# Kernel optimization log

Measured on AMD Instinct MI355X. Metric: run time of the kernel, lower is better.

## Reference

```python
import jax, jax.numpy as jnp
import numpy as np

H = 8        # heads
DH = 64      # dim_head
IMG = 32     # image_size
KS = 5       # kernel_size (odd)
SCALE = DH ** -0.5


def _unfold(t, ks):
    # t: (b, c, Hp, Wp) already padded. Returns (b, c*ks*ks, Ho*Wo) with
    # channel-major layout (c outermost, then kh, kw) matching torch F.unfold.
    b, c, Hp, Wp = t.shape
    Ho, Wo = Hp - ks + 1, Wp - ks + 1
    pat = jnp.stack([t[:, :, i:i + Ho, j:j + Wo]
                     for i in range(ks) for j in range(ks)], axis=2)  # (b,c,ks*ks,Ho,Wo)
    return pat.reshape(b, c * ks * ks, Ho * Wo)


def setup_inputs() -> dict:
    key = jax.random.key(0)
    k1, k2, k3, k4 = jax.random.split(key, 4)
    b, n, dim, inner = 2, 1152, 512, 512
    x = jax.random.normal(k1, (b, n, dim), jnp.float32)
    w_qkv = jax.random.normal(k2, (dim, inner * 3), jnp.float32) * 0.02
    w_out = jax.random.normal(k3, (inner, dim), jnp.float32) * 0.02
    b_out = jax.random.normal(k4, (dim,), jnp.float32) * 0.02
    return {"x": x, "w_qkv": w_qkv, "w_out": w_out, "b_out": b_out}


def reference(x, w_qkv, w_out, b_out):
    b, n, dim = x.shape
    img_len = IMG * IMG
    text_len = n - img_len
    NEG = -jnp.finfo(x.dtype).max

    qkv = x @ w_qkv                                   # (b, n, 3*inner)
    q, k, v = jnp.split(qkv, 3, axis=-1)

    def to_heads(t):
        return t.reshape(b, n, H, DH).transpose(0, 2, 1, 3).reshape(b * H, n, DH)

    q = to_heads(q) * SCALE
    k = to_heads(k)
    v = to_heads(v)

    # faithful to source: text slice is t[:, img_seq_len:], image is t[:, -img_seq_len:]
    q_text, q_img = q[:, img_len:], q[:, -img_len:]
    k_text, k_img = k[:, img_len:], k[:, -img_len:]
    v_text, v_img = v[:, img_len:], v[:, -img_len:]

    # ---- text branch. NOTE: source uses non-inplace masked_fill, so the
    # causal mask has NO effect -> plain softmax (faithful reproduction).
    dots_text = jnp.einsum('bid,bjd->bij', q_text, k_text)
    attn_text = jax.nn.softmax(dots_text, axis=-1)
    out_text = jnp.einsum('bij,bjd->bid', attn_text, v_text)

    # ---- image branch: local window via unfold
    def to_loc(t):
        g = t.transpose(0, 2, 1).reshape(b * H, DH, IMG, IMG)
        p = KS // 2
        g = jnp.pad(g, ((0, 0), (0, 0), (p, p), (p, p)))
        u = _unfold(g, KS)  # (bh, DH*KS*KS, img_len), channel-major (d outer)
        # faithful to source rearrange 'b (j d) i -> b i j d' (j outermost),
        # which regroups the channel-major unfold output.
        return u.reshape(b * H, KS * KS, DH, img_len).transpose(0, 3, 1, 2)

    k_loc = to_loc(k_img)  # (bh, img_len, KS*KS, DH)
    v_loc = to_loc(v_img)

    dots_txt = jnp.einsum('bid,bjd->bij', q_img, k_text)     # (bh, img_len, text_len)
    dots_loc = jnp.einsum('bid,bijd->bij', q_img, k_loc)     # (bh, img_len, KS*KS)

    # per-query key index mask (padded positions get index img_len -> never masked)
    p = KS // 2
    idx = jnp.arange(img_len, dtype=jnp.float32).reshape(1, 1, IMG, IMG)
    idx = jnp.pad(idx, ((0, 0), (0, 0), (p, p), (p, p)), constant_values=float(img_len))
    kidx = _unfold(idx, KS).transpose(0, 2, 1)               # (1, img_len, KS*KS)
    qidx = jnp.arange(img_len, dtype=jnp.float32).reshape(1, -1, 1)
    mask_loc = qidx <= kidx                                  # faithful: keep q <= k
    dots_loc = jnp.where(mask_loc, dots_loc, NEG)

    dots_img = jnp.concatenate([dots_txt, dots_loc], axis=-1)
    attn_img = jax.nn.softmax(dots_img, axis=-1)
    out_img = (jnp.einsum('bij,bjd->bid', attn_img[..., :text_len], v_text)
               + jnp.einsum('bij,bijd->bid', attn_img[..., text_len:], v_loc))

    out = jnp.concatenate([out_text, out_img], axis=1)       # (bh, n, DH)
    out = out.reshape(b, H, n, DH).transpose(0, 2, 1, 3).reshape(b, n, H * DH)
    return out @ w_out + b_out
```

## Files before the change

kernel.cpp:

```cpp
#include <hip/hip_runtime.h>
#include <hip/hip_bf16.h>
#include <math.h>

#define NTOK 1152
#define DIM 512
#define NQKV 1536
#define DHEAD 64
#define NBH 16
#define TEXTN 128
#define IMGLEN 1024
#define SEG (NBH * NTOK * DHEAD)
#define STF 68
#define TSTATE_F (NBH * IMGLEN * STF)
#define LPAD 40
#define KTSZ (NBH * TEXTN * DHEAD)

typedef __attribute__((ext_vector_type(8))) short bf16x8;
typedef __attribute__((ext_vector_type(8))) ushort u16x8;
typedef __attribute__((ext_vector_type(4))) float f32x4;

__device__ __forceinline__ ushort f2bf(float f) {
    unsigned u = __float_as_uint(f);
    unsigned r = (u + 0x7FFFu + ((u >> 16) & 1u)) >> 16;
    return (ushort)r;
}
__device__ __forceinline__ float bf2f(ushort u) {
    return __uint_as_float(((unsigned)u) << 16);
}

__global__ __launch_bounds__(256) void prep_x_k(const float* __restrict__ X,
                                                ushort* __restrict__ xhi,
                                                ushort* __restrict__ xlo) {
    int i = (blockIdx.x * 256 + threadIdx.x) * 4;
    float4 v = *(const float4*)(X + i);
    ushort4 h, l;
    h.x = f2bf(v.x); l.x = f2bf(v.x - bf2f(h.x));
    h.y = f2bf(v.y); l.y = f2bf(v.y - bf2f(h.y));
    h.z = f2bf(v.z); l.z = f2bf(v.z - bf2f(h.z));
    h.w = f2bf(v.w); l.w = f2bf(v.w - bf2f(h.w));
    *(ushort4*)(xhi + i) = h;
    *(ushort4*)(xlo + i) = l;
}

__global__ __launch_bounds__(256) void prep_wt_k(const float* __restrict__ W,
                                                 ushort* __restrict__ thi,
                                                 ushort* __restrict__ tlo,
                                                 int K, int N) {
    __shared__ float tile[32][33];
    const int bx = blockIdx.x, by = blockIdx.y;
    const int c = threadIdx.x & 31, r8 = threadIdx.x >> 5;
#pragma unroll
    for (int i = 0; i < 4; ++i) {
        int rr = r8 + i * 8;
        tile[rr][c] = W[(size_t)(by * 32 + rr) * N + bx * 32 + c];
    }
    __syncthreads();
#pragma unroll
    for (int i = 0; i < 4; ++i) {
        int rr = r8 + i * 8;
        float v = tile[c][rr];
        size_t o = (size_t)(bx * 32 + rr) * K + by * 32 + c;
        ushort h = f2bf(v);
        thi[o] = h;
        tlo[o] = f2bf(v - bf2f(h));
    }
}

__global__ __launch_bounds__(256) void gemm_qkv_mfma(const ushort* __restrict__ xhi,
                                                     const ushort* __restrict__ xlo,
                                                     const ushort* __restrict__ wthi,
                                                     const ushort* __restrict__ wtlo,
                                                     float* __restrict__ qh,
                                                     float* __restrict__ kh,
                                                     float* __restrict__ vh,
                                                     ushort* __restrict__ qhi,
                                                     ushort* __restrict__ qlo,
                                                     ushort* __restrict__ kthi,
                                                     ushort* __restrict__ ktlo,
                                                     ushort* __restrict__ vthi,
                                                     ushort* __restrict__ vtlo) {
    __shared__ __align__(16) ushort Ah[128 * LPAD], Al[128 * LPAD];
    __shared__ __align__(16) ushort Bh[64 * LPAD], Bl[64 * LPAD];
    __shared__ __align__(16) float Cb[128 * 68];
    const int tid = threadIdx.x;
    const int lane = tid & 63;
    const int w = tid >> 6;
    const int wm = w >> 1, wn = w & 1;
    const int row0 = blockIdx.y * 128;
    const int col0 = blockIdx.x * 64;

    f32x4 acc[4][2];
#pragma unroll
    for (int a = 0; a < 4; ++a)
#pragma unroll
        for (int b = 0; b < 2; ++b) acc[a][b] = (f32x4){0.f, 0.f, 0.f, 0.f};

    const int arow = tid >> 1;
    const int akb = (tid & 1) * 16;
    const int brow = tid >> 2;
    const int bkb = (tid & 3) * 8;
    const int kf = (lane >> 4) * 8;
    const int lr = lane & 15;
    const int lg = lane >> 4;

    for (int k0 = 0; k0 < DIM; k0 += 32) {
        {
            const size_t g = (size_t)(row0 + arow) * DIM + k0 + akb;
            *(bf16x8*)&Ah[arow * LPAD + akb] = *(const bf16x8*)(xhi + g);
            *(bf16x8*)&Ah[arow * LPAD + akb + 8] = *(const bf16x8*)(xhi + g + 8);
            *(bf16x8*)&Al[arow * LPAD + akb] = *(const bf16x8*)(xlo + g);
            *(bf16x8*)&Al[arow * LPAD + akb + 8] = *(const bf16x8*)(xlo + g + 8);
        }
        {
            const size_t g = (size_t)(col0 + brow) * DIM + k0 + bkb;
            *(bf16x8*)&Bh[brow * LPAD + bkb] = *(const bf16x8*)(wthi + g);
            *(bf16x8*)&Bl[brow * LPAD + bkb] = *(const bf16x8*)(wtlo + g);
        }
        __syncthreads();
        bf16x8 ah[4], al[4], bh[2], bl[2];
#pragma unroll
        for (int mi = 0; mi < 4; ++mi) {
            int rr = wm * 64 + mi * 16 + lr;
            ah[mi] = *(const bf16x8*)&Ah[rr * LPAD + kf];
            al[mi] = *(const bf16x8*)&Al[rr * LPAD + kf];
        }
#pragma unroll
        for (int ni = 0; ni < 2; ++ni) {
            int rr = wn * 32 + ni * 16 + lr;
            bh[ni] = *(const bf16x8*)&Bh[rr * LPAD + kf];
            bl[ni] = *(const bf16x8*)&Bl[rr * LPAD + kf];
        }
#pragma unroll
        for (int mi = 0; mi < 4; ++mi)
#pragma unroll
            for (int ni = 0; ni < 2; ++ni) {
                acc[mi][ni] = __builtin_amdgcn_mfma_f32_16x16x32_bf16(ah[mi], bh[ni], acc[mi][ni], 0, 0, 0);
                acc[mi][ni] = __builtin_amdgcn_mfma_f32_16x16x32_bf16(ah[mi], bl[ni], acc[mi][ni], 0, 0, 0);
                acc[mi][ni] = __builtin_amdgcn_mfma_f32_16x16x32_bf16(al[mi], bh[ni], acc[mi][ni], 0, 0, 0);
            }
        __syncthreads();
    }

#pragma unroll
    for (int mi = 0; mi < 4; ++mi)
#pragma unroll
        for (int ni = 0; ni < 2; ++ni)
#pragma unroll
            for (int j = 0; j < 4; ++j) {
                int lrow = wm * 64 + mi * 16 + lg * 4 + j;
                int lcol = wn * 32 + ni * 16 + lr;
                Cb[lrow * 68 + lcol] = acc[mi][ni][j];
            }
    __syncthreads();

    const int which = col0 >> 9;
    const int hh = (col0 & 511) >> 6;
    const float scale = (which == 0) ? 0.125f : 1.f;
    float* dst = (which == 0) ? qh : ((which == 1) ? kh : vh);

    const int orow = tid >> 1;
    const int och = (tid & 1) * 32;
    const int r = row0 + orow;
    const int b_i = r / NTOK, tok = r - b_i * NTOK;
    const int bhi = b_i * 8 + hh;

    float vals[32];
#pragma unroll
    for (int g = 0; g < 8; ++g) {
        float4 v = *(const float4*)&Cb[orow * 68 + och + g * 4];
        vals[g * 4] = v.x * scale; vals[g * 4 + 1] = v.y * scale;
        vals[g * 4 + 2] = v.z * scale; vals[g * 4 + 3] = v.w * scale;
    }
    {
        float* dp = dst + ((size_t)bhi * NTOK + tok) * DHEAD + och;
#pragma unroll
        for (int g = 0; g < 8; ++g) {
            float4 o;
            o.x = vals[g * 4]; o.y = vals[g * 4 + 1];
            o.z = vals[g * 4 + 2]; o.w = vals[g * 4 + 3];
            *(float4*)(dp + g * 4) = o;
        }
    }
    if (which == 0) {
        size_t qo = ((size_t)bhi * NTOK + tok) * DHEAD + och;
        u16x8 h8[2], l8[2];
#pragma unroll
        for (int h2 = 0; h2 < 2; ++h2)
#pragma unroll
            for (int e = 0; e < 8; ++e) {
                float v = vals[h2 * 8 + e + (h2 ? 8 : 0)];
                (void)v;
            }
#pragma unroll
        for (int half = 0; half < 2; ++half) {
            u16x8 hh8, ll8;
#pragma unroll
            for (int e = 0; e < 8; ++e) {
                float v = vals[half * 16 + e];
                ushort hv = f2bf(v);
                hh8[e] = hv; ll8[e] = f2bf(v - bf2f(hv));
            }
            *(u16x8*)(qhi + qo + half * 16) = hh8;
            *(u16x8*)(qlo + qo + half * 16) = ll8;
            u16x8 hh9, ll9;
#pragma unroll
            for (int e = 0; e < 8; ++e) {
                float v = vals[half * 16 + 8 + e];
                ushort hv = f2bf(v);
                hh9[e] = hv; ll9[e] = f2bf(v - bf2f(hv));
            }
            *(u16x8*)(qhi + qo + half * 16 + 8) = hh9;
            *(u16x8*)(qlo + qo + half * 16 + 8) = ll9;
        }
    } else if (tok >= IMGLEN) {
        const int tr = tok - IMGLEN;
        if (which == 1) {
            size_t ko = ((size_t)bhi * TEXTN + tr) * DHEAD + och;
#pragma unroll
            for (int half = 0; half < 4; ++half) {
                u16x8 hh8, ll8;
#pragma unroll
                for (int e = 0; e < 8; ++e) {
                    float v = vals[half * 8 + e];
                    ushort hv = f2bf(v);
                    hh8[e] = hv; ll8[e] = f2bf(v - bf2f(hv));
                }
                *(u16x8*)(kthi + ko + half * 8) = hh8;
                *(u16x8*)(ktlo + ko + half * 8) = ll8;
            }
        } else {
#pragma unroll
            for (int e = 0; e < 32; ++e) {
                int d = och + e;
                size_t vo = ((size_t)bhi * DHEAD + d) * TEXTN + tr;
                ushort hv = f2bf(vals[e]);
                vthi[vo] = hv;
                vtlo[vo] = f2bf(vals[e] - bf2f(hv));
            }
        }
    }
}

__global__ __launch_bounds__(256) void attn_text_mfma(const ushort* __restrict__ qhi,
                                                      const ushort* __restrict__ qlo,
                                                      const ushort* __restrict__ kthi,
                                                      const ushort* __restrict__ ktlo,
                                                      const ushort* __restrict__ vthi,
                                                      const ushort* __restrict__ vtlo,
                                                      ushort* __restrict__ ahi,
                                                      ushort* __restrict__ alo,
                                                      float* __restrict__ tstate) {
    __shared__ __align__(16) ushort Phi[4][16][136];
    __shared__ __align__(16) ushort Plo[4][16][136];
    const int bh = blockIdx.x / 18;
    const int tile = blockIdx.x % 18;
    const int wave = threadIdx.x >> 6;
    const int lane = threadIdx.x & 63;
    const int lr = lane & 15, lg = lane >> 4;
    const int kf = lg * 8;
    const int qrow0 = tile * 64 + wave * 16;
    const int tok0 = (tile < 2 ? 1024 + tile * 64 : tile * 64) + wave * 16;

    bf16x8 qah[2], qal[2];
    {
        const size_t qb = ((size_t)bh * NTOK + tok0 + lr) * DHEAD;
#pragma unroll
        for (int c = 0; c < 2; ++c) {
            qah[c] = *(const bf16x8*)(qhi + qb + c * 32 + kf);
            qal[c] = *(const bf16x8*)(qlo + qb + c * 32 + kf);
        }
    }
    f32x4 s[8];
#pragma unroll
    for (int t = 0; t < 8; ++t) s[t] = (f32x4){0.f, 0.f, 0.f, 0.f};
#pragma unroll
    for (int t = 0; t < 8; ++t) {
        const size_t kb = ((size_t)bh * TEXTN + t * 16 + lr) * DHEAD;
#pragma unroll
        for (int c = 0; c < 2; ++c) {
            bf16x8 kbh = *(const bf16x8*)(kthi + kb + c * 32 + kf);
            bf16x8 kbl = *(const bf16x8*)(ktlo + kb + c * 32 + kf);
            s[t] = __builtin_amdgcn_mfma_f32_16x16x32_bf16(qah[c], kbh, s[t], 0, 0, 0);
            s[t] = __builtin_amdgcn_mfma_f32_16x16x32_bf16(qah[c], kbl, s[t], 0, 0, 0);
            s[t] = __builtin_amdgcn_mfma_f32_16x16x32_bf16(qal[c], kbh, s[t], 0, 0, 0);
        }
    }
    float mx[4], sm[4];
#pragma unroll
    for (int r = 0; r < 4; ++r) {
        float v = s[0][r];
#pragma unroll
        for (int t = 1; t < 8; ++t) v = fmaxf(v, s[t][r]);
        mx[r] = v;
    }
#pragma unroll
    for (int msk = 1; msk <= 8; msk <<= 1)
#pragma unroll
        for (int r = 0; r < 4; ++r) mx[r] = fmaxf(mx[r], __shfl_xor(mx[r], msk));
#pragma unroll
    for (int r = 0; r < 4; ++r) sm[r] = 0.f;
#pragma unroll
    for (int t = 0; t < 8; ++t)
#pragma unroll
        for (int r = 0; r < 4; ++r) {
            float p = __expf(s[t][r] - mx[r]);
            s[t][r] = p;
            sm[r] += p;
        }
#pragma unroll
    for (int msk = 1; msk <= 8; msk <<= 1)
#pragma unroll
        for (int r = 0; r < 4; ++r) sm[r] += __shfl_xor(sm[r], msk);
#pragma unroll
    for (int t = 0; t < 8; ++t)
#pragma unroll
        for (int r = 0; r < 4; ++r) {
            float p = s[t][r];
            ushort h = f2bf(p);
            Phi[wave][lg * 4 + r][t * 16 + lr] = h;
            Plo[wave][lg * 4 + r][t * 16 + lr] = f2bf(p - bf2f(h));
        }
    __syncthreads();
    f32x4 o[4];
#pragma unroll
    for (int dt = 0; dt < 4; ++dt) o[dt] = (f32x4){0.f, 0.f, 0.f, 0.f};
#pragma unroll
    for (int c = 0; c < 4; ++c) {
        bf16x8 pah = *(const bf16x8*)&Phi[wave][lr][c * 32 + kf];
        bf16x8 pal = *(const bf16x8*)&Plo[wave][lr][c * 32 + kf];
#pragma unroll
        for (int dt = 0; dt < 4; ++dt) {
            const size_t vb = ((size_t)bh * DHEAD + dt * 16 + lr) * TEXTN + c * 32 + kf;
            bf16x8 vbh = *(const bf16x8*)(vthi + vb);
            bf16x8 vbl = *(const bf16x8*)(vtlo + vb);
            o[dt] = __builtin_amdgcn_mfma_f32_16x16x32_bf16(pah, vbh, o[dt], 0, 0, 0);
            o[dt] = __builtin_amdgcn_mfma_f32_16x16x32_bf16(pah, vbl, o[dt], 0, 0, 0);
            o[dt] = __builtin_amdgcn_mfma_f32_16x16x32_bf16(pal, vbh, o[dt], 0, 0, 0);
        }
    }
    if (tile < 2) {
#pragma unroll
        for (int r = 0; r < 4; ++r) {
            const int row = qrow0 + lg * 4 + r;
            const float inv = 1.f / sm[r];
            const size_t base = ((size_t)bh * NTOK + row) * DHEAD;
#pragma unroll
            for (int dt = 0; dt < 4; ++dt) {
                float v = o[dt][r] * inv;
                ushort h = f2bf(v);
                ahi[base + dt * 16 + lr] = h;
                alo[base + dt * 16 + lr] = f2bf(v - bf2f(h));
            }
        }
    } else {
#pragma unroll
        for (int r = 0; r < 4; ++r) {
            const int imgq = qrow0 - TEXTN + lg * 4 + r;
            float* st = tstate + ((size_t)bh * IMGLEN + imgq) * STF;
#pragma unroll
            for (int dt = 0; dt < 4; ++dt) st[dt * 16 + lr] = o[dt][r];
            if (lr == 0) { st[64] = mx[r]; st[65] = sm[r]; }
        }
    }
}

template <int W8>
__device__ inline void loc_dots8_lds(const float* __restrict__ Kl, int yloc, int x, int y,
                                     const float (&q)[64], float (&sd)[25]) {
#pragma unroll
    for (int t = 0; t < 25; ++t) {
        const int ny = y + t / 5 - 2;
        const int nx = x + t % 5 - 2;
        if (ny >= 0 && ny < 32 && nx >= 0 && nx < 32) {
            const int px = (yloc + t / 5) * 32 + nx;
            const float* base = Kl + px * 64;
            float4 k0 = *(const float4*)(base + (((2 * W8) ^ (px & 7)) << 2));
            float4 k1 = *(const float4*)(base + (((2 * W8 + 1) ^ (px & 7)) << 2));
            float ke[8] = {k0.x, k0.y, k0.z, k0.w, k1.x, k1.y, k1.z, k1.w};
#pragma unroll
            for (int e = 0; e < 8; ++e) {
                const int d = W8 * 8 + e;
                const int id2 = d * 25 + t;
                sd[id2 >> 6] += q[id2 & 63] * ke[e];
            }
        }
    }
}

template <int W, int T0, int T1>
__device__ inline void loc_pvr_lds(const float* __restrict__ Vl, int yloc, int x, int y,
                                   const float (&pp)[25], float (&po)[64]) {
#pragma unroll
    for (int t = T0; t < T1; ++t) {
        const int ny = y + t / 5 - 2;
        const int nx = x + t % 5 - 2;
        if (ny >= 0 && ny < 32 && nx >= 0 && nx < 32) {
            const int px = (yloc + t / 5) * 32 + nx;
            const float* base = Vl + px * 64;
#pragma unroll
            for (int g = 0; g < 4; ++g) {
                float4 vv = *(const float4*)(base + (((4 * W + g) ^ (px & 7)) << 2));
                float ve[4] = {vv.x, vv.y, vv.z, vv.w};
#pragma unroll
                for (int e = 0; e < 4; ++e) {
                    const int d = W * 16 + g * 4 + e;
                    const int id2 = d * 25 + t;
                    po[id2 & 63] += pp[id2 >> 6] * ve[e];
                }
            }
        }
    }
}

__global__ __launch_bounds__(512, 1) void attn_img_k(const float* __restrict__ qh,
                                                     const float* __restrict__ kh,
                                                     const float* __restrict__ vh,
                                                     ushort* __restrict__ ahi,
                                                     ushort* __restrict__ alo,
                                                     const float* __restrict__ tstate) {
    __shared__ __align__(16) float smem[8 * 64 * 26];
    __shared__ __align__(16) float Kl[192 * 64];
    __shared__ __align__(16) float Vl[192 * 64];
    float (*sdb)[64][26] = reinterpret_cast<float (*)[64][26]>(smem);
    float (*pob)[64][68] = reinterpret_cast<float (*)[64][68]>(smem);
    const int bh = blockIdx.x >> 4;
    const int qtile = (blockIdx.x & 15) << 6;
    const int yr0 = qtile >> 5;
    const int wave = threadIdx.x >> 6;
    const int lane = threadIdx.x & 63;
    const int qq = qtile + lane;
    const int y = qq >> 5, x = qq & 31;
    const int yloc = lane >> 5;
    const float* kimg = kh + (size_t)(bh * NTOK + TEXTN) * DHEAD;
    const float* vimg = vh + (size_t)(bh * NTOK + TEXTN) * DHEAD;
    const float* st = tstate + ((size_t)(bh * IMGLEN + qq)) * STF;

#pragma unroll
    for (int i = 0; i < 6; ++i) {
        int flat = threadIdx.x + i * 512;
        int px = flat >> 4, b = flat & 15;
        int gy = yr0 - 2 + (px >> 5), gx = px & 31;
        if (gy >= 0 && gy < 32) {
            size_t off = ((size_t)(gy * 32 + gx)) * DHEAD + b * 4;
            int dsto = px * 64 + ((b ^ (px & 7)) << 2);
            *(float4*)&Kl[dsto] = *(const float4*)(kimg + off);
            *(float4*)&Vl[dsto] = *(const float4*)(vimg + off);
        }
    }
    {
        const float* qbase = qh + ((size_t)(bh * NTOK + TEXTN + qtile)) * DHEAD;
#pragma unroll
        for (int i = 0; i < 2; ++i) {
            int flat = threadIdx.x + i * 512;
            int px = flat >> 4, b = flat & 15;
            *(float4*)&smem[px * 64 + ((b ^ (px & 7)) << 2)] =
                *(const float4*)(qbase + (size_t)px * DHEAD + b * 4);
        }
    }
    __syncthreads();

    float q[64];
#pragma unroll
    for (int b = 0; b < 16; ++b) {
        float4 v = *(const float4*)&smem[lane * 64 + ((b ^ (lane & 7)) << 2)];
        q[b * 4] = v.x; q[b * 4 + 1] = v.y; q[b * 4 + 2] = v.z; q[b * 4 + 3] = v.w;
    }
    __syncthreads();

    float sd[25];
#pragma unroll
    for (int j = 0; j < 25; ++j) sd[j] = 0.f;
    switch (wave) {
        case 0: loc_dots8_lds<0>(Kl, yloc, x, y, q, sd); break;
        case 1: loc_dots8_lds<1>(Kl, yloc, x, y, q, sd); break;
        case 2: loc_dots8_lds<2>(Kl, yloc, x, y, q, sd); break;
        case 3: loc_dots8_lds<3>(Kl, yloc, x, y, q, sd); break;
        case 4: loc_dots8_lds<4>(Kl, yloc, x, y, q, sd); break;
        case 5: loc_dots8_lds<5>(Kl, yloc, x, y, q, sd); break;
        case 6: loc_dots8_lds<6>(Kl, yloc, x, y, q, sd); break;
        default: loc_dots8_lds<7>(Kl, yloc, x, y, q, sd); break;
    }
#pragma unroll
    for (int j = 0; j < 25; ++j) sdb[wave][lane][j] = sd[j];
    __syncthreads();

    float p[25];
#pragma unroll
    for (int j = 0; j < 25; ++j)
        p[j] = ((sdb[0][lane][j] + sdb[1][lane][j]) + (sdb[2][lane][j] + sdb[3][lane][j])) +
               ((sdb[4][lane][j] + sdb[5][lane][j]) + (sdb[6][lane][j] + sdb[7][lane][j]));
    float m = st[64], l = st[65];
    float mloc = -1e30f;
#pragma unroll
    for (int j = 0; j < 25; ++j) {
        const int my = y + j / 5 - 2;
        const int mx2 = x + j % 5 - 2;
        bool inb = (my >= 0 && my < 32 && mx2 >= 0 && mx2 < 32);
        bool keep = inb ? (qq <= my * 32 + mx2) : true;
        p[j] = keep ? p[j] : -1e30f;
        mloc = fmaxf(mloc, p[j]);
    }
    const float M = fmaxf(m, mloc);
    const float cc = __expf(m - M);
    l *= cc;
#pragma unroll
    for (int j = 0; j < 25; ++j) {
        p[j] = __expf(p[j] - M);
        l += p[j];
    }
    const float inv = 1.f / l;

    float po[64];
#pragma unroll
    for (int o = 0; o < 64; ++o) po[o] = 0.f;
    switch (wave) {
        case 0: loc_pvr_lds<0, 0, 13>(Vl, yloc, x, y, p, po); break;
        case 1: loc_pvr_lds<1, 0, 13>(Vl, yloc, x, y, p, po); break;
        case 2: loc_pvr_lds<2, 0, 13>(Vl, yloc, x, y, p, po); break;
        case 3: loc_pvr_lds<3, 0, 13>(Vl, yloc, x, y, p, po); break;
        case 4: loc_pvr_lds<0, 13, 25>(Vl, yloc, x, y, p, po); break;
        case 5: loc_pvr_lds<1, 13, 25>(Vl, yloc, x, y, p, po); break;
        case 6: loc_pvr_lds<2, 13, 25>(Vl, yloc, x, y, p, po); break;
        default: loc_pvr_lds<3, 13, 25>(Vl, yloc, x, y, p, po); break;
    }
    __syncthreads();

    if (wave < 2) {
#pragma unroll
        for (int o = 0; o < 64; ++o) pob[wave][lane][o] = po[o];
    }
    __syncthreads();
    if (wave >= 2 && wave < 4) {
#pragma unroll
        for (int o = 0; o < 64; ++o) pob[wave - 2][lane][o] += po[o];
    }
    __syncthreads();
    if (wave >= 4 && wave < 6) {
#pragma unroll
        for (int o = 0; o < 64; ++o) pob[wave - 4][lane][o] += po[o];
    }
    __syncthreads();
    if (wave >= 6) {
#pragma unroll
        for (int o = 0; o < 64; ++o) pob[wave - 6][lane][o] += po[o];
    }
    __syncthreads();

    if (wave < 4) {
        const float* stq = st + wave * 16;
        size_t base = ((size_t)(bh * NTOK + TEXTN + qq)) * DHEAD + wave * 16;
#pragma unroll
        for (int g = 0; g < 4; ++g) {
            float4 tv = *(const float4*)(stq + g * 4);
            float4 a0 = *(const float4*)&pob[0][lane][wave * 16 + g * 4];
            float4 a1 = *(const float4*)&pob[1][lane][wave * 16 + g * 4];
            float v0 = (a0.x + a1.x + cc * tv.x) * inv;
            float v1 = (a0.y + a1.y + cc * tv.y) * inv;
            float v2 = (a0.z + a1.z + cc * tv.z) * inv;
            float v3 = (a0.w + a1.w + cc * tv.w) * inv;
            ushort4 oh, ol;
            oh.x = f2bf(v0); ol.x = f2bf(v0 - bf2f(oh.x));
            oh.y = f2bf(v1); ol.y = f2bf(v1 - bf2f(oh.y));
            oh.z = f2bf(v2); ol.z = f2bf(v2 - bf2f(oh.z));
            oh.w = f2bf(v3); ol.w = f2bf(v3 - bf2f(oh.w));
            *(ushort4*)(ahi + base + g * 4) = oh;
            *(ushort4*)(alo + base + g * 4) = ol;
        }
    }
}

__global__ __launch_bounds__(256) void gemm_out_mfma(const ushort* __restrict__ ahi,
                                                     const ushort* __restrict__ alo,
                                                     const ushort* __restrict__ wthi,
                                                     const ushort* __restrict__ wtlo,
                                                     const float* __restrict__ bias,
                                                     float* __restrict__ Y) {
    __shared__ __align__(16) ushort Ah[128 * LPAD], Al[128 * LPAD];
    __shared__ __align__(16) ushort Bh[64 * LPAD], Bl[64 * LPAD];
    __shared__ __align__(16) float Cb[128 * 68];
    const int tid = threadIdx.x;
    const int lane = tid & 63;
    const int w = tid >> 6;
    const int wm = w >> 1, wn = w & 1;
    const int row0 = blockIdx.y * 128;
    const int col0 = blockIdx.x * 64;

    f32x4 acc[4][2];
#pragma unroll
    for (int a = 0; a < 4; ++a)
#pragma unroll
        for (int b = 0; b < 2; ++b) acc[a][b] = (f32x4){0.f, 0.f, 0.f, 0.f};

    const int arow = tid >> 1;
    const int akb = (tid & 1) * 16;
    const int brow = tid >> 2;
    const int bkb = (tid & 3) * 8;
    const int kf = (lane >> 4) * 8;
    const int lr = lane & 15;
    const int lg = lane >> 4;

    const int ar = row0 + arow;
    const int a_bi = ar / NTOK;
    const int a_tok = ar - a_bi * NTOK;

    for (int k0 = 0; k0 < DIM; k0 += 32) {
        {
            const int kg = k0 + akb;
            const int hh = kg >> 6, d0 = kg & 63;
            const size_t g = ((size_t)(a_bi * 8 + hh) * NTOK + a_tok) * DHEAD + d0;
            *(bf16x8*)&Ah[arow * LPAD + akb] = *(const bf16x8*)(ahi + g);
            *(bf16x8*)&Ah[arow * LPAD + akb + 8] = *(const bf16x8*)(ahi + g + 8);
            *(bf16x8*)&Al[arow * LPAD + akb] = *(const bf16x8*)(alo + g);
            *(bf16x8*)&Al[arow * LPAD + akb + 8] = *(const bf16x8*)(alo + g + 8);
        }
        {
            const size_t g = (size_t)(col0 + brow) * DIM + k0 + bkb;
            *(bf16x8*)&Bh[brow * LPAD + bkb] = *(const bf16x8*)(wthi + g);
            *(bf16x8*)&Bl[brow * LPAD + bkb] = *(const bf16x8*)(wtlo + g);
        }
        __syncthreads();
        bf16x8 ah[4], al[4], bh[2], bl[2];
#pragma unroll
        for (int mi = 0; mi < 4; ++mi) {
            int rr = wm * 64 + mi * 16 + lr;
            ah[mi] = *(const bf16x8*)&Ah[rr * LPAD + kf];
            al[mi] = *(const bf16x8*)&Al[rr * LPAD + kf];
        }
#pragma unroll
        for (int ni = 0; ni < 2; ++ni) {
            int rr = wn * 32 + ni * 16 + lr;
            bh[ni] = *(const bf16x8*)&Bh[rr * LPAD + kf];
            bl[ni] = *(const bf16x8*)&Bl[rr * LPAD + kf];
        }
#pragma unroll
        for (int mi = 0; mi < 4; ++mi)
#pragma unroll
            for (int ni = 0; ni < 2; ++ni) {
                acc[mi][ni] = __builtin_amdgcn_mfma_f32_16x16x32_bf16(ah[mi], bh[ni], acc[mi][ni], 0, 0, 0);
                acc[mi][ni] = __builtin_amdgcn_mfma_f32_16x16x32_bf16(ah[mi], bl[ni], acc[mi][ni], 0, 0, 0);
                acc[mi][ni] = __builtin_amdgcn_mfma_f32_16x16x32_bf16(al[mi], bh[ni], acc[mi][ni], 0, 0, 0);
            }
        __syncthreads();
    }

#pragma unroll
    for (int mi = 0; mi < 4; ++mi)
#pragma unroll
        for (int ni = 0; ni < 2; ++ni)
#pragma unroll
            for (int j = 0; j < 4; ++j) {
                int lrow = wm * 64 + mi * 16 + lg * 4 + j;
                int lcol = wn * 32 + ni * 16 + lr;
                Cb[lrow * 68 + lcol] = acc[mi][ni][j];
            }
    __syncthreads();

    const int orow = tid >> 1;
    const int och = (tid & 1) * 32;
    const int r = row0 + orow;
    float* yp = Y + (size_t)r * DIM + col0 + och;
    const float* bp = bias + col0 + och;
#pragma unroll
    for (int g = 0; g < 8; ++g) {
        float4 v = *(const float4*)&Cb[orow * 68 + och + g * 4];
        float4 b = *(const float4*)(bp + g * 4);
        float4 o;
        o.x = v.x + b.x; o.y = v.y + b.y; o.z = v.z + b.z; o.w = v.w + b.w;
        *(float4*)(yp + g * 4) = o;
    }
}

extern "C" void kernel_launch(void* const* d_in, const int* in_sizes, int n_in,
                              void* d_out, int out_size, void* d_ws, size_t ws_size,
                              hipStream_t stream) {
    const float* x = (const float*)d_in[0];
    const float* w_qkv = (const float*)d_in[1];
    const float* w_out = (const float*)d_in[2];
    const float* b_out = (const float*)d_in[3];
    float* Y = (float*)d_out;
    float* ws = (float*)d_ws;
    float* qh = ws;
    float* kh = ws + (size_t)SEG;
    float* vh = ws + 2 * (size_t)SEG;
    float* tstate = ws + 3 * (size_t)SEG;
    ushort* xhi = (ushort*)(ws + 3 * (size_t)SEG + TSTATE_F);
    ushort* xlo = xhi + (size_t)SEG;
    ushort* ahi = xhi;
    ushort* alo = xlo;
    ushort* wqthi = xlo + (size_t)SEG;
    ushort* wqtlo = wqthi + (size_t)DIM * NQKV;
    ushort* wothi = wqtlo + (size_t)DIM * NQKV;
    ushort* wotlo = wothi + (size_t)DIM * DIM;
    ushort* qhi = wotlo + (size_t)DIM * DIM;
    ushort* qlo = qhi + (size_t)SEG;
    ushort* kthi = qlo + (size_t)SEG;
    ushort* ktlo = kthi + (size_t)KTSZ;
    ushort* vthi = ktlo + (size_t)KTSZ;
    ushort* vtlo = vthi + (size_t)KTSZ;

    hipLaunchKernelGGL(prep_x_k, dim3(SEG / 1024), dim3(256), 0, stream, x, xhi, xlo);
    hipLaunchKernelGGL(prep_wt_k, dim3(NQKV / 32, DIM / 32), dim3(256), 0, stream,
                       w_qkv, wqthi, wqtlo, DIM, NQKV);
    hipLaunchKernelGGL(prep_wt_k, dim3(DIM / 32, DIM / 32), dim3(256), 0, stream,
                       w_out, wothi, wotlo, DIM, DIM);
    hipLaunchKernelGGL(gemm_qkv_mfma, dim3(NQKV / 64, 2304 / 128), dim3(256), 0, stream,
                       xhi, xlo, wqthi, wqtlo, qh, kh, vh,
                       qhi, qlo, kthi, ktlo, vthi, vtlo);
    hipLaunchKernelGGL(attn_text_mfma, dim3(NBH * 18), dim3(256), 0, stream,
                       qhi, qlo, kthi, ktlo, vthi, vtlo, ahi, alo, tstate);
    hipLaunchKernelGGL(attn_img_k, dim3(NBH * 16), dim3(512), 0, stream,
                       qh, kh, vh, ahi, alo, tstate);
    hipLaunchKernelGGL(gemm_out_mfma, dim3(DIM / 64, 2304 / 128), dim3(256), 0, stream,
                       ahi, alo, wothi, wotlo, b_out, Y);
}
```

Before: 125.7 us.

## Collapse image-attention kernel to one wave per block, dropping cross-wave reductions

Rewrites the local-window image attention so a single 64-thread wave handles each 64-query tile and computes every head dimension itself. Before, eight waves split the head dimension and combined partial dot products and outputs through shared-memory reductions with many barriers. This removes the LDS reduction traffic and the barriers, but each block now has 8x fewer threads for the global-to-LDS loads. Each thread also does 8x more serial FMA work, with large register arrays (q, sd, out), on only 256 single-wave blocks, which leaves the GPU with little parallelism.

```diff
diff --git a/kernel.cpp b/kernel.cpp
--- a/kernel.cpp
+++ b/kernel.cpp
@@ -183,14 +183,6 @@
     }
     if (which == 0) {
         size_t qo = ((size_t)bhi * NTOK + tok) * DHEAD + och;
-        u16x8 h8[2], l8[2];
-#pragma unroll
-        for (int h2 = 0; h2 < 2; ++h2)
-#pragma unroll
-            for (int e = 0; e < 8; ++e) {
-                float v = vals[h2 * 8 + e + (h2 ? 8 : 0)];
-                (void)v;
-            }
 #pragma unroll
         for (int half = 0; half < 2; ++half) {
             u16x8 hh8, ll8;
@@ -364,70 +356,19 @@
     }
 }
 
-template <int W8>
-__device__ inline void loc_dots8_lds(const float* __restrict__ Kl, int yloc, int x, int y,
-                                     const float (&q)[64], float (&sd)[25]) {
-#pragma unroll
-    for (int t = 0; t < 25; ++t) {
-        const int ny = y + t / 5 - 2;
-        const int nx = x + t % 5 - 2;
-        if (ny >= 0 && ny < 32 && nx >= 0 && nx < 32) {
-            const int px = (yloc + t / 5) * 32 + nx;
-            const float* base = Kl + px * 64;
-            float4 k0 = *(const float4*)(base + (((2 * W8) ^ (px & 7)) << 2));
-            float4 k1 = *(const float4*)(base + (((2 * W8 + 1) ^ (px & 7)) << 2));
-            float ke[8] = {k0.x, k0.y, k0.z, k0.w, k1.x, k1.y, k1.z, k1.w};
-#pragma unroll
-            for (int e = 0; e < 8; ++e) {
-                const int d = W8 * 8 + e;
-                const int id2 = d * 25 + t;
-                sd[id2 >> 6] += q[id2 & 63] * ke[e];
-            }
-        }
-    }
-}
-
-template <int W, int T0, int T1>
-__device__ inline void loc_pvr_lds(const float* __restrict__ Vl, int yloc, int x, int y,
-                                   const float (&pp)[25], float (&po)[64]) {
-#pragma unroll
-    for (int t = T0; t < T1; ++t) {
-        const int ny = y + t / 5 - 2;
-        const int nx = x + t % 5 - 2;
-        if (ny >= 0 && ny < 32 && nx >= 0 && nx < 32) {
-            const int px = (yloc + t / 5) * 32 + nx;
-            const float* base = Vl + px * 64;
-#pragma unroll
-            for (int g = 0; g < 4; ++g) {
-                float4 vv = *(const float4*)(base + (((4 * W + g) ^ (px & 7)) << 2));
-                float ve[4] = {vv.x, vv.y, vv.z, vv.w};
-#pragma unroll
-                for (int e = 0; e < 4; ++e) {
-                    const int d = W * 16 + g * 4 + e;
-                    const int id2 = d * 25 + t;
-                    po[id2 & 63] += pp[id2 >> 6] * ve[e];
-                }
-            }
-        }
-    }
-}
-
-__global__ __launch_bounds__(512, 1) void attn_img_k(const float* __restrict__ qh,
-                                                     const float* __restrict__ kh,
-                                                     const float* __restrict__ vh,
-                                                     ushort* __restrict__ ahi,
-                                                     ushort* __restrict__ alo,
-                                                     const float* __restrict__ tstate) {
-    __shared__ __align__(16) float smem[8 * 64 * 26];
+__global__ __launch_bounds__(64, 1) void attn_img_k(const float* __restrict__ qh,
+                                                    const float* __restrict__ kh,
+                                                    const float* __restrict__ vh,
+                                                    ushort* __restrict__ ahi,
+                                                    ushort* __restrict__ alo,
+                                                    const float* __restrict__ tstate) {
     __shared__ __align__(16) float Kl[192 * 64];
     __shared__ __align__(16) float Vl[192 * 64];
-    float (*sdb)[64][26] = reinterpret_cast<float (*)[64][26]>(smem);
-    float (*pob)[64][68] = reinterpret_cast<float (*)[64][68]>(smem);
+    __shared__ __align__(16) float Qb[64 * 64];
     const int bh = blockIdx.x >> 4;
     const int qtile = (blockIdx.x & 15) << 6;
     const int yr0 = qtile >> 5;
-    const int wave = threadIdx.x >> 6;
-    const int lane = threadIdx.x & 63;
+    const int lane = threadIdx.x;
     const int qq = qtile + lane;
     const int y = qq >> 5, x = qq & 31;
     const int yloc = lane >> 5;
@@ -435,9 +376,8 @@
     const float* vimg = vh + (size_t)(bh * NTOK + TEXTN) * DHEAD;
     const float* st = tstate + ((size_t)(bh * IMGLEN + qq)) * STF;
 
-#pragma unroll
-    for (int i = 0; i < 6; ++i) {
-        int flat = threadIdx.x + i * 512;
+    for (int i = 0; i < 48; ++i) {
+        int flat = lane + i * 64;
         int px = flat >> 4, b = flat & 15;
         int gy = yr0 - 2 + (px >> 5), gx = px & 31;
         if (gy >= 0 && gy < 32) {
@@ -449,11 +389,10 @@
     }
     {
         const float* qbase = qh + ((size_t)(bh * NTOK + TEXTN + qtile)) * DHEAD;
-#pragma unroll
-        for (int i = 0; i < 2; ++i) {
-            int flat = threadIdx.x + i * 512;
+        for (int i = 0; i < 16; ++i) {
+            int flat = lane + i * 64;
             int px = flat >> 4, b = flat & 15;
-            *(float4*)&smem[px * 64 + ((b ^ (px & 7)) << 2)] =
+            *(float4*)&Qb[px * 64 + ((b ^ (px & 7)) << 2)] =
                 *(const float4*)(qbase + (size_t)px * DHEAD + b * 4);
         }
     }
@@ -462,33 +401,34 @@
     float q[64];
 #pragma unroll
     for (int b = 0; b < 16; ++b) {
-        float4 v = *(const float4*)&smem[lane * 64 + ((b ^ (lane & 7)) << 2)];
+        float4 v = *(const float4*)&Qb[lane * 64 + ((b ^ (lane & 7)) << 2)];
         q[b * 4] = v.x; q[b * 4 + 1] = v.y; q[b * 4 + 2] = v.z; q[b * 4 + 3] = v.w;
     }
-    __syncthreads();
 
     float sd[25];
 #pragma unroll
     for (int j = 0; j < 25; ++j) sd[j] = 0.f;
-    switch (wave) {
-        case 0: loc_dots8_lds<0>(Kl, yloc, x, y, q, sd); break;
-        case 1: loc_dots8_lds<1>(Kl, yloc, x, y, q, sd); break;
-        case 2: loc_dots8_lds<2>(Kl, yloc, x, y, q, sd); break;
-        case 3: loc_dots8_lds<3>(Kl, yloc, x, y, q, sd); break;
-        case 4: loc_dots8_lds<4>(Kl, yloc, x, y, q, sd); break;
-        case 5: loc_dots8_lds<5>(Kl, yloc, x, y, q, sd); break;
-        case 6: loc_dots8_lds<6>(Kl, yloc, x, y, q, sd); break;
-        default: loc_dots8_lds<7>(Kl, yloc, x, y, q, sd); break;
-    }
-#pragma unroll
-    for (int j = 0; j < 25; ++j) sdb[wave][lane][j] = sd[j];
-    __syncthreads();
-
-    float p[25];
-#pragma unroll
-    for (int j = 0; j < 25; ++j)
-        p[j] = ((sdb[0][lane][j] + sdb[1][lane][j]) + (sdb[2][lane][j] + sdb[3][lane][j])) +
-               ((sdb[4][lane][j] + sdb[5][lane][j]) + (sdb[6][lane][j] + sdb[7][lane][j]));
+#pragma unroll
+    for (int t = 0; t < 25; ++t) {
+        const int ny = y + t / 5 - 2;
+        const int nx = x + t % 5 - 2;
+        if (ny >= 0 && ny < 32 && nx >= 0 && nx < 32) {
+            const int px = (yloc + t / 5) * 32 + nx;
+            const float* base = Kl + px * 64;
+#pragma unroll
+            for (int b16 = 0; b16 < 16; ++b16) {
+                float4 kv = *(const float4*)(base + ((b16 ^ (px & 7)) << 2));
+                float ke[4] = {kv.x, kv.y, kv.z, kv.w};
+#pragma unroll
+                for (int e = 0; e < 4; ++e) {
+                    const int d = b16 * 4 + e;
+                    const int id2 = d * 25 + t;
+                    sd[id2 >> 6] += q[id2 & 63] * ke[e];
+                }
+            }
+        }
+    }
+
     float m = st[64], l = st[65];
     float mloc = -1e30f;
 #pragma unroll
@@ -497,75 +437,61 @@
         const int mx2 = x + j % 5 - 2;
         bool inb = (my >= 0 && my < 32 && mx2 >= 0 && mx2 < 32);
         bool keep = inb ? (qq <= my * 32 + mx2) : true;
-        p[j] = keep ? p[j] : -1e30f;
-        mloc = fmaxf(mloc, p[j]);
+        sd[j] = keep ? sd[j] : -1e30f;
+        mloc = fmaxf(mloc, sd[j]);
     }
     const float M = fmaxf(m, mloc);
     const float cc = __expf(m - M);
     l *= cc;
 #pragma unroll
     for (int j = 0; j < 25; ++j) {
-        p[j] = __expf(p[j] - M);
-        l += p[j];
+        sd[j] = __expf(sd[j] - M);
+        l += sd[j];
     }
     const float inv = 1.f / l;
 
-    float po[64];
-#pragma unroll
-    for (int o = 0; o < 64; ++o) po[o] = 0.f;
-    switch (wave) {
-        case 0: loc_pvr_lds<0, 0, 13>(Vl, yloc, x, y, p, po); break;
-        case 1: loc_pvr_lds<1, 0, 13>(Vl, yloc, x, y, p, po); break;
-        case 2: loc_pvr_lds<2, 0, 13>(Vl, yloc, x, y, p, po); break;
-        case 3: loc_pvr_lds<3, 0, 13>(Vl, yloc, x, y, p, po); break;
-        case 4: loc_pvr_lds<0, 13, 25>(Vl, yloc, x, y, p, po); break;
-        case 5: loc_pvr_lds<1, 13, 25>(Vl, yloc, x, y, p, po); break;
-        case 6: loc_pvr_lds<2, 13, 25>(Vl, yloc, x, y, p, po); break;
-        default: loc_pvr_lds<3, 13, 25>(Vl, yloc, x, y, p, po); break;
-    }
-    __syncthreads();
-
-    if (wave < 2) {
-#pragma unroll
-        for (int o = 0; o < 64; ++o) pob[wave][lane][o] = po[o];
-    }
-    __syncthreads();
-    if (wave >= 2 && wave < 4) {
-#pragma unroll
-        for (int o = 0; o < 64; ++o) pob[wave - 2][lane][o] += po[o];
-    }
-    __syncthreads();
-    if (wave >= 4 && wave < 6) {
-#pragma unroll
-        for (int o = 0; o < 64; ++o) pob[wave - 4][lane][o] += po[o];
-    }
-    __syncthreads();
-    if (wave >= 6) {
-#pragma unroll
-        for (int o = 0; o < 64; ++o) pob[wave - 6][lane][o] += po[o];
-    }
-    __syncthreads();
-
-    if (wave < 4) {
-        const float* stq = st + wave * 16;
-        size_t base = ((size_t)(bh * NTOK + TEXTN + qq)) * DHEAD + wave * 16;
-#pragma unroll
-        for (int g = 0; g < 4; ++g) {
-            float4 tv = *(const float4*)(stq + g * 4);
-            float4 a0 = *(const float4*)&pob[0][lane][wave * 16 + g * 4];
-            float4 a1 = *(const float4*)&pob[1][lane][wave * 16 + g * 4];
-            float v0 = (a0.x + a1.x + cc * tv.x) * inv;
-            float v1 = (a0.y + a1.y + cc * tv.y) * inv;
-            float v2 = (a0.z + a1.z + cc * tv.z) * inv;
-            float v3 = (a0.w + a1.w + cc * tv.w) * inv;
-            ushort4 oh, ol;
-            oh.x = f2bf(v0); ol.x = f2bf(v0 - bf2f(oh.x));
-            oh.y = f2bf(v1); ol.y = f2bf(v1 - bf2f(oh.y));
-            oh.z = f2bf(v2); ol.z = f2bf(v2 - bf2f(oh.z));
-            oh.w = f2bf(v3); ol.w = f2bf(v3 - bf2f(oh.w));
-            *(ushort4*)(ahi + base + g * 4) = oh;
-            *(ushort4*)(alo + base + g * 4) = ol;
-        }
+    float out[64];
+#pragma unroll
+    for (int g = 0; g < 16; ++g) {
+        float4 tv = *(const float4*)(st + g * 4);
+        out[g * 4] = cc * tv.x; out[g * 4 + 1] = cc * tv.y;
+        out[g * 4 + 2] = cc * tv.z; out[g * 4 + 3] = cc * tv.w;
+    }
+#pragma unroll
+    for (int t = 0; t < 25; ++t) {
+        const int ny = y + t / 5 - 2;
+        const int nx = x + t % 5 - 2;
+        if (ny >= 0 && ny < 32 && nx >= 0 && nx < 32) {
+            const int px = (yloc + t / 5) * 32 + nx;
+            const float* base = Vl + px * 64;
+#pragma unroll
+            for (int b16 = 0; b16 < 16; ++b16) {
+                float4 vv = *(const float4*)(base + ((b16 ^ (px & 7)) << 2));
+                float ve[4] = {vv.x, vv.y, vv.z, vv.w};
+#pragma unroll
+                for (int e = 0; e < 4; ++e) {
+                    const int d = b16 * 4 + e;
+                    const int id2 = d * 25 + t;
+                    out[id2 & 63] += sd[id2 >> 6] * ve[e];
+                }
+            }
+        }
+    }
+
+    const size_t base = ((size_t)(bh * NTOK + TEXTN + qq)) * DHEAD;
+#pragma unroll
+    for (int g = 0; g < 16; ++g) {
+        float v0 = out[g * 4] * inv;
+        float v1 = out[g * 4 + 1] * inv;
+        float v2 = out[g * 4 + 2] * inv;
+        float v3 = out[g * 4 + 3] * inv;
+        ushort4 oh, ol;
+        oh.x = f2bf(v0); ol.x = f2bf(v0 - bf2f(oh.x));
+        oh.y = f2bf(v1); ol.y = f2bf(v1 - bf2f(oh.y));
+        oh.z = f2bf(v2); ol.z = f2bf(v2 - bf2f(oh.z));
+        oh.w = f2bf(v3); ol.w = f2bf(v3 - bf2f(oh.w));
+        *(ushort4*)(ahi + base + g * 4) = oh;
+        *(ushort4*)(alo + base + g * 4) = ol;
     }
 }
 
@@ -708,7 +634,7 @@
                        qhi, qlo, kthi, ktlo, vthi, vtlo);
     hipLaunchKernelGGL(attn_text_mfma, dim3(NBH * 18), dim3(256), 0, stream,
                        qhi, qlo, kthi, ktlo, vthi, vtlo, ahi, alo, tstate);
-    hipLaunchKernelGGL(attn_img_k, dim3(NBH * 16), dim3(512), 0, stream,
+    hipLaunchKernelGGL(attn_img_k, dim3(NBH * 16), dim3(64), 0, stream,
                        qh, kh, vh, ahi, alo, tstate);
     hipLaunchKernelGGL(gemm_out_mfma, dim3(DIM / 64, 2304 / 128), dim3(256), 0, stream,
                        ahi, alo, wothi, wotlo, b_out, Y);
```

Measured after the change: 141.8 us. 1.13x slower.
